# Optimization experiments

Hardware: AMD Instinct MI355X
Metric: run time of the kernel (lower is better)

## Reference

```python
import jax, jax.numpy as jnp
import numpy as np

N_EMBD = 2048
N_HEAD = 16
N_INNER = 8192
EPS = 1e-5


def _wn_weight(v, g):
    # torch weight_norm with dim=1 on weight [out, in]:
    # w[:, j] = g[j] * v[:, j] / ||v[:, j]||_2
    norm = jnp.sqrt(jnp.sum(v * v, axis=0))  # [in]
    return v * (g / norm)[None, :]


def _layer_norm(x, gamma, beta):
    mu = jnp.mean(x, axis=-1, keepdims=True)
    var = jnp.mean(jnp.square(x - mu), axis=-1, keepdims=True)
    return (x - mu) * jax.lax.rsqrt(var + EPS) * gamma + beta


def setup_inputs() -> dict:
    key = jax.random.key(0)
    ks = jax.random.split(key, 12)
    E, I, H = N_EMBD, N_INNER, N_HEAD
    s = lambda n: 1.0 / np.sqrt(n)
    return {
        "hidden_states": jax.random.normal(ks[0], (2, 2048, E), jnp.float32),
        "ln1_g": jnp.ones((E,), jnp.float32),
        "ln1_b": jnp.zeros((E,), jnp.float32),
        "w_qkv": jax.random.normal(ks[1], (3 * E, E), jnp.float32) * s(E),
        "b_qkv": jnp.zeros((3 * E,), jnp.float32),
        "attn_proj_v": jax.random.normal(ks[2], (E, E), jnp.float32) * s(E),
        "attn_proj_g": jnp.abs(jax.random.normal(ks[3], (E,), jnp.float32)) + 0.5,
        "attn_proj_b": jnp.zeros((E,), jnp.float32),
        "emotion_bias": jax.random.normal(ks[4], (H,), jnp.float32) * 0.1,
        "ln2_g": jnp.ones((E,), jnp.float32),
        "ln2_b": jnp.zeros((E,), jnp.float32),
        "w_fc": jax.random.normal(ks[5], (I, E), jnp.float32) * s(E),
        "b_fc": jnp.zeros((I,), jnp.float32),
        "mlp_proj_v": jax.random.normal(ks[6], (E, I), jnp.float32) * s(I),
        "mlp_proj_g": jnp.abs(jax.random.normal(ks[7], (I,), jnp.float32)) + 0.5,
        "mlp_proj_b": jnp.zeros((E,), jnp.float32),
    }


def reference(hidden_states, ln1_g, ln1_b, w_qkv, b_qkv, attn_proj_v, attn_proj_g,
              attn_proj_b, emotion_bias, ln2_g, ln2_b, w_fc, b_fc,
              mlp_proj_v, mlp_proj_g, mlp_proj_b):
    B, S, E = hidden_states.shape
    H = N_HEAD
    D = E // H

    # --- attention sub-block ---
    residual = hidden_states
    x = _layer_norm(hidden_states, ln1_g, ln1_b)
    qkv = x @ w_qkv.T + b_qkv                       # [B,S,3E]
    q, k, v = jnp.split(qkv, 3, axis=-1)
    q = q.reshape(B, S, H, D).transpose(0, 2, 1, 3)  # [B,H,S,D]
    k = k.reshape(B, S, H, D).transpose(0, 2, 1, 3)
    v = v.reshape(B, S, H, D).transpose(0, 2, 1, 3)

    scores = jnp.einsum("bhqd,bhkd->bhqk", q, k) / jnp.sqrt(jnp.float32(D))
    scores = scores + emotion_bias[None, :, None, None]
    probs = jax.nn.softmax(scores, axis=-1)
    attn = jnp.einsum("bhqk,bhkd->bhqd", probs, v)   # [B,H,S,D]
    attn = attn.transpose(0, 2, 1, 3).reshape(B, S, E)
    w_proj = _wn_weight(attn_proj_v, attn_proj_g)
    attn = attn @ w_proj.T + attn_proj_b

    hidden = attn + residual

    # --- MLP sub-block ---
    residual = hidden
    x = _layer_norm(hidden, ln2_g, ln2_b)
    h = jax.nn.gelu(x @ w_fc.T + b_fc, approximate=False)
    w_proj2 = _wn_weight(mlp_proj_v, mlp_proj_g)
    h = h @ w_proj2.T + mlp_proj_b
    return residual + h
```

## Files before the change

kernel.cpp:

```cpp
#include <hip/hip_runtime.h>
#include <hip/hip_bf16.h>

#define DEVI __device__ __forceinline__

typedef __attribute__((ext_vector_type(8))) __bf16 bf16x8;
typedef __attribute__((ext_vector_type(4))) float f32x4;
typedef __attribute__((ext_vector_type(4))) unsigned short u16x4;
typedef __attribute__((ext_vector_type(8))) unsigned short u16x8;

DEVI unsigned short f2bf(float f) {
  unsigned int u = __float_as_uint(f);
  u += 0x7FFFu + ((u >> 16) & 1u);
  return (unsigned short)(u >> 16);
}
DEVI float bf2f(unsigned short u) {
  return __uint_as_float(((unsigned int)u) << 16);
}

#define GLD16(g, l) __builtin_amdgcn_global_load_lds(                      \
    (const __attribute__((address_space(1))) void*)(g),                    \
    (__attribute__((address_space(3))) void*)(l), 16, 0, 0)


__global__ __launch_bounds__(256) void cast_k(const float* __restrict__ in,
                                              unsigned short* __restrict__ out,
                                              int n4) {
  for (int i = blockIdx.x * 256 + threadIdx.x; i < n4; i += gridDim.x * 256) {
    f32x4 v = ((const f32x4*)in)[i];
    u16x4 o;
    o.x = f2bf(v.x); o.y = f2bf(v.y); o.z = f2bf(v.z); o.w = f2bf(v.w);
    ((u16x4*)out)[i] = o;
  }
}

__global__ __launch_bounds__(256) void colnorm1_k(const float* __restrict__ v,
                                                  float* __restrict__ part,
                                                  int cols) {
  const int tid = threadIdx.x;
  const int g = tid & 127;
  const int s = tid >> 7;
  const int c0 = blockIdx.x * 512;
  const int r0 = blockIdx.y * 64 + s * 32;
  const float* base = v + (size_t)r0 * cols + c0 + g * 4;
  f32x4 acc = {};
#pragma unroll 4
  for (int i = 0; i < 32; ++i) {
    f32x4 x = *(const f32x4*)(base + (size_t)i * cols);
    acc.x += x.x * x.x; acc.y += x.y * x.y;
    acc.z += x.z * x.z; acc.w += x.w * x.w;
  }
  __shared__ f32x4 red[256];
  red[tid] = acc;
  __syncthreads();
  if (s == 0) {
    f32x4 a = red[tid], b = red[tid + 128];
    f32x4 o;
    o.x = a.x + b.x; o.y = a.y + b.y; o.z = a.z + b.z; o.w = a.w + b.w;
    *(f32x4*)(part + (size_t)blockIdx.y * cols + c0 + g * 4) = o;
  }
}

__global__ __launch_bounds__(256) void colnorm2_k(const float* __restrict__ part,
                                                  const float* __restrict__ g,
                                                  float* __restrict__ s,
                                                  int cols, int nrc) {
  const int c = blockIdx.x * 256 + threadIdx.x;
  float acc = 0.f;
  for (int i = 0; i < nrc; ++i) acc += part[(size_t)i * cols + c];
  s[c] = g[c] * rsqrtf(acc);
}

__global__ __launch_bounds__(256) void scale_cast_k(const float* __restrict__ in,
                                                    const float* __restrict__ s,
                                                    unsigned short* __restrict__ out,
                                                    int cols, int n4) {
  const int cmask4 = (cols >> 2) - 1;
  for (int i = blockIdx.x * 256 + threadIdx.x; i < n4; i += gridDim.x * 256) {
    f32x4 v = ((const f32x4*)in)[i];
    f32x4 sv = ((const f32x4*)s)[i & cmask4];
    u16x4 o;
    o.x = f2bf(v.x * sv.x); o.y = f2bf(v.y * sv.y);
    o.z = f2bf(v.z * sv.z); o.w = f2bf(v.w * sv.w);
    ((u16x4*)out)[i] = o;
  }
}

__global__ __launch_bounds__(256) void ln_k(const float* __restrict__ x,
                                            const float* __restrict__ g,
                                            const float* __restrict__ b,
                                            unsigned short* __restrict__ out) {
  const int tid = threadIdx.x, lane = tid & 63, wid = tid >> 6;
  const int row = blockIdx.x;
  const float* xr = x + (size_t)row * 2048;
  f32x4 a0 = ((const f32x4*)xr)[tid];
  f32x4 a1 = ((const f32x4*)xr)[tid + 256];
  float s = a0.x + a0.y + a0.z + a0.w + a1.x + a1.y + a1.z + a1.w;
  float ss = a0.x * a0.x + a0.y * a0.y + a0.z * a0.z + a0.w * a0.w +
             a1.x * a1.x + a1.y * a1.y + a1.z * a1.z + a1.w * a1.w;
#pragma unroll
  for (int m = 1; m < 64; m <<= 1) {
    s += __shfl_xor(s, m);
    ss += __shfl_xor(ss, m);
  }
  __shared__ float red[8];
  if (lane == 0) { red[wid] = s; red[4 + wid] = ss; }
  __syncthreads();
  s = red[0] + red[1] + red[2] + red[3];
  ss = red[4] + red[5] + red[6] + red[7];
  const float mu = s * (1.f / 2048.f);
  const float var = ss * (1.f / 2048.f) - mu * mu;
  const float rs = rsqrtf(var + 1e-5f);
  f32x4 g0 = ((const f32x4*)g)[tid], g1 = ((const f32x4*)g)[tid + 256];
  f32x4 b0 = ((const f32x4*)b)[tid], b1 = ((const f32x4*)b)[tid + 256];
  u16x4 o0, o1;
  o0.x = f2bf((a0.x - mu) * rs * g0.x + b0.x);
  o0.y = f2bf((a0.y - mu) * rs * g0.y + b0.y);
  o0.z = f2bf((a0.z - mu) * rs * g0.z + b0.z);
  o0.w = f2bf((a0.w - mu) * rs * g0.w + b0.w);
  o1.x = f2bf((a1.x - mu) * rs * g1.x + b1.x);
  o1.y = f2bf((a1.y - mu) * rs * g1.y + b1.y);
  o1.z = f2bf((a1.z - mu) * rs * g1.z + b1.z);
  o1.w = f2bf((a1.w - mu) * rs * g1.w + b1.w);
  unsigned short* orow = out + (size_t)row * 2048;
  *(u16x4*)(orow + 4 * tid) = o0;
  *(u16x4*)(orow + 1024 + 4 * tid) = o1;
}

__global__ __launch_bounds__(256) void vtrans_k(const unsigned short* __restrict__ qkv,
                                                unsigned short* __restrict__ vt) {
  __shared__ unsigned short t[64][134];
  const int tid = threadIdx.x;
  const int bh = blockIdx.x >> 5, st = blockIdx.x & 31;
  const int b = bh >> 4, h = bh & 15;
  const unsigned short* vb = qkv + (size_t)(b * 2048 + st * 64) * 6144 + 4096 + h * 128;
#pragma unroll
  for (int i = 0; i < 4; ++i) {
    int f = tid + (i << 8);
    int row = f >> 4, c8 = f & 15;
    u16x8 x = *(const u16x8*)(vb + (size_t)row * 6144 + c8 * 8);
#pragma unroll
    for (int j = 0; j < 4; ++j) {
      unsigned int pk = ((unsigned int)x[2 * j + 1] << 16) | x[2 * j];
      *(unsigned int*)&t[row][c8 * 8 + 2 * j] = pk;
    }
  }
  __syncthreads();
  const int lane = tid & 63, wid = tid >> 6;
  unsigned short* ob = vt + ((size_t)bh << 18) + (st << 6);
#pragma unroll
  for (int j = 0; j < 32; ++j) {
    int d = (wid << 5) + j;
    ob[((size_t)d << 11) + lane] = t[lane][d];
  }
}

__global__ __launch_bounds__(256) void g4red_k(const unsigned short* __restrict__ parts,
                                               const float* __restrict__ bias,
                                               const float* __restrict__ res,
                                               float* __restrict__ out, int n4) {
  const size_t PS = (size_t)4096 * 2048;
  for (int i = blockIdx.x * 256 + threadIdx.x; i < n4; i += gridDim.x * 256) {
    u16x4 a = ((const u16x4*)(parts))[i];
    u16x4 b = ((const u16x4*)(parts + PS))[i];
    u16x4 c = ((const u16x4*)(parts + 2 * PS))[i];
    u16x4 d = ((const u16x4*)(parts + 3 * PS))[i];
    f32x4 r = ((const f32x4*)res)[i];
    f32x4 bb = ((const f32x4*)bias)[i & 511];
    f32x4 o;
    o.x = bf2f(a.x) + bf2f(b.x) + bf2f(c.x) + bf2f(d.x) + r.x + bb.x;
    o.y = bf2f(a.y) + bf2f(b.y) + bf2f(c.y) + bf2f(d.y) + r.y + bb.y;
    o.z = bf2f(a.z) + bf2f(b.z) + bf2f(c.z) + bf2f(d.z) + r.z + bb.z;
    o.w = bf2f(a.w) + bf2f(b.w) + bf2f(c.w) + bf2f(d.w) + r.w + bb.w;
    ((f32x4*)out)[i] = o;
  }
}

struct GemmP {
  const unsigned short* A;
  const unsigned short* B;
  const float* bias;
  const float* res;
  float* outF;
  unsigned short* outH;
  int M, N, K;
};

DEVI void gemm128_body(const GemmP& p, int m0, int n0, int k0, int nk) {
  const int tid = threadIdx.x, lane = tid & 63, wid = tid >> 6;
  const int K = p.K;
  const int wr = wid >> 1, wc = wid & 1;

  __shared__ __align__(16) unsigned short sA[2][4096];
  __shared__ __align__(16) unsigned short sB[2][4096];

  const int c0 = tid, c1 = tid + 256;
  const unsigned short* gA0 = p.A + (size_t)(m0 + (c0 >> 2)) * K + k0 + ((c0 & 3) << 3);
  const unsigned short* gA1 = p.A + (size_t)(m0 + (c1 >> 2)) * K + k0 + ((c1 & 3) << 3);
  const unsigned short* gB0 = p.B + (size_t)(n0 + (c0 >> 2)) * K + k0 + ((c0 & 3) << 3);
  const unsigned short* gB1 = p.B + (size_t)(n0 + (c1 >> 2)) * K + k0 + ((c1 & 3) << 3);
  const int l0 = wid << 9, l1 = (wid << 9) + 2048;

  f32x4 acc[4][4] = {};
  const int arow = (wr << 6) + (lane & 15);
  const int brow = (wc << 6) + (lane & 15);
  const int koff = (lane >> 4) << 3;

#define STAGE128(bufi, t) do { int ko = (t) << 5;       \
    GLD16(gA0 + ko, &sA[bufi][l0]);                     \
    GLD16(gA1 + ko, &sA[bufi][l1]);                     \
    GLD16(gB0 + ko, &sB[bufi][l0]);                     \
    GLD16(gB1 + ko, &sB[bufi][l1]); } while (0)

  STAGE128(0, 0);
  __syncthreads();
  int cur = 0;
  for (int t = 0; t < nk; ++t) {
    if (t + 1 < nk) STAGE128(cur ^ 1, t + 1);
    bf16x8 af[4], bfr[4];
#pragma unroll
    for (int i = 0; i < 4; ++i)
      af[i] = *(const bf16x8*)&sA[cur][(arow + (i << 4)) * 32 + koff];
#pragma unroll
    for (int i = 0; i < 4; ++i)
      bfr[i] = *(const bf16x8*)&sB[cur][(brow + (i << 4)) * 32 + koff];
#pragma unroll
    for (int i = 0; i < 4; ++i)
#pragma unroll
      for (int j = 0; j < 4; ++j)
        acc[i][j] = __builtin_amdgcn_mfma_f32_16x16x32_bf16(af[i], bfr[j], acc[i][j], 0, 0, 0);
    __syncthreads();
    cur ^= 1;
  }
#undef STAGE128

  const int rbase = m0 + (wr << 6) + ((lane >> 4) << 2);
  const int cbase = n0 + (wc << 6) + (lane & 15);
#pragma unroll
  for (int mi = 0; mi < 4; ++mi) {
#pragma unroll
    for (int ni = 0; ni < 4; ++ni) {
      const int col = cbase + (ni << 4);
#pragma unroll
      for (int r = 0; r < 4; ++r) {
        const int row = rbase + (mi << 4) + r;
        const size_t o = (size_t)row * p.N + col;
        p.outF[o] = acc[mi][ni][r] + p.bias[col] + p.res[o];
      }
    }
  }
}

__global__ __launch_bounds__(256) void g2_proj128(GemmP p) {
  const int x = blockIdx.x & 7, i = blockIdx.x >> 3;
  const int bm = (x >> 1) * 8 + (i >> 3);
  const int bn = (x & 1) * 8 + (i & 7);
  gemm128_body(p, bm << 7, bn << 7, 0, p.K >> 5);
}

DEVI void setup256(const GemmP& p, int m0, int n0, int k0,
                   const unsigned short*& gsA0, const unsigned short*& gsA1,
                   const unsigned short*& gsB0, const unsigned short*& gsB1) {
  const int tid = threadIdx.x;
  int r_[2], c_[2];
#pragma unroll
  for (int j = 0; j < 2; ++j) {
    int d = tid * 16 + j * 8192;
    int w = (d & 1023) ^ (((d >> 9) & 1) << 5);
    r_[j] = ((d >> 10) << 4) + (w >> 6);
    c_[j] = (w & 63) >> 1;
  }
  gsA0 = p.A + (size_t)(m0 + r_[0]) * p.K + k0 + c_[0];
  gsA1 = p.A + (size_t)(m0 + r_[1]) * p.K + k0 + c_[1];
  gsB0 = p.B + (size_t)(n0 + r_[0]) * p.K + k0 + c_[0];
  gsB1 = p.B + (size_t)(n0 + r_[1]) * p.K + k0 + c_[1];
}

template <int EPI>
DEVI void epi256(const GemmP& p, f32x4 (&acc)[8][4], int m0, int n0,
                 unsigned short* outH) {
  const int lane = threadIdx.x & 63, wid = threadIdx.x >> 6;
  const int wr = wid >> 2, wc = wid & 3;
  const int lr = lane & 15, lk = lane >> 4;
  const int rbase = m0 + wr * 128 + (lk << 2);
  const int cbase = n0 + wc * 64 + lr;
#pragma unroll
  for (int m = 0; m < 8; ++m) {
#pragma unroll
    for (int n = 0; n < 4; ++n) {
      const int col = cbase + (n << 4);
      const float bb = (EPI == 5) ? 0.f : p.bias[col];
#pragma unroll
      for (int r = 0; r < 4; ++r) {
        const int row = rbase + (m << 4) + r;
        float v = acc[m][n][r] + bb;
        if constexpr (EPI == 2) {
          float y = 0.7978845608028654f * (v + 0.044715f * v * v * v);
          float u = __expf(2.f * y);
          v = (y > 40.f) ? v : v * (u / (u + 1.f));
        }
        outH[(size_t)row * p.N + col] = f2bf(v);
      }
    }
  }
}

template <int EPI>
DEVI void gemm2p_body(const GemmP& p, unsigned short* lds_raw, int m0, int n0,
                      int k0, int nk, unsigned short* outH) {
  const int tid = threadIdx.x, lane = tid & 63, wid = tid >> 6;
  const int wr = wid >> 2, wc = wid & 3;
  const int lr = lane & 15, lk = lane >> 4;
  const int fb = (lr * 64 + lk * 16) ^ ((lr & 8) << 2);

  const unsigned short *gsA0, *gsA1, *gsB0, *gsB1;
  setup256(p, m0, n0, k0, gsA0, gsA1, gsB0, gsB1);

#define STG2(b, kt) do { unsigned short* _d = lds_raw + ((b) << 14);     \
    GLD16(gsA0 + ((size_t)(kt) << 5), _d + (tid << 3));                  \
    GLD16(gsA1 + ((size_t)(kt) << 5), _d + 4096 + (tid << 3));           \
    GLD16(gsB0 + ((size_t)(kt) << 5), _d + 8192 + (tid << 3));           \
    GLD16(gsB1 + ((size_t)(kt) << 5), _d + 12288 + (tid << 3)); } while (0)

  f32x4 acc[8][4] = {};
  STG2(0, 0);
  __syncthreads();
  int cur = 0;
  for (int t = 0; t < nk; ++t) {
    if (t + 1 < nk) STG2(cur ^ 1, t + 1);
    const char* tA = (const char*)(lds_raw + (cur << 14));
    const char* tB = tA + 16384;
    bf16x8 a_[8], b_[4];
#pragma unroll
    for (int n = 0; n < 4; ++n)
      b_[n] = *(const bf16x8*)(tB + (((wc << 2) + n) << 10) + fb);
#pragma unroll
    for (int m = 0; m < 8; ++m)
      a_[m] = *(const bf16x8*)(tA + (((wr << 3) + m) << 10) + fb);
#pragma unroll
    for (int m = 0; m < 8; ++m)
#pragma unroll
      for (int n = 0; n < 4; ++n)
        acc[m][n] = __builtin_amdgcn_mfma_f32_16x16x32_bf16(a_[m], b_[n], acc[m][n], 0, 0, 0);
    __syncthreads();
    cur ^= 1;
  }
#undef STG2
  epi256<EPI>(p, acc, m0, n0, outH);
}

template <int EPI>
DEVI void gemmr4_body(const GemmP& p, unsigned short* lds_raw, int m0, int n0,
                      int k0, int nk, unsigned short* outH) {
  const int tid = threadIdx.x, lane = tid & 63, wid = tid >> 6;
  const int wr = wid >> 2, wc = wid & 3;
  const int lr = lane & 15, lk = lane >> 4;
  const int fb = (lr * 64 + lk * 16) ^ ((lr & 8) << 2);

  const unsigned short *gsA0, *gsA1, *gsB0, *gsB1;
  setup256(p, m0, n0, k0, gsA0, gsA1, gsB0, gsB1);

#define STGR(bufi, kt) do { unsigned short* _d = lds_raw + ((bufi) << 14); \
    GLD16(gsA0 + ((size_t)(kt) << 5), _d + (tid << 3));                    \
    GLD16(gsA1 + ((size_t)(kt) << 5), _d + 4096 + (tid << 3));             \
    GLD16(gsB0 + ((size_t)(kt) << 5), _d + 8192 + (tid << 3));             \
    GLD16(gsB1 + ((size_t)(kt) << 5), _d + 12288 + (tid << 3)); } while (0)

  f32x4 acc[8][4] = {};
  STGR(0, 0);
  STGR(1, 1);
  STGR(2, 2);
  asm volatile("s_waitcnt vmcnt(8)" ::: "memory");
  __builtin_amdgcn_s_barrier();
  asm volatile("" ::: "memory");

  for (int t = 0; t < nk; ++t) {
    const char* tA = (const char*)(lds_raw + ((t & 3) << 14));
    const char* tB = tA + 16384;
    bf16x8 a_[8], b_[4];
#pragma unroll
    for (int n = 0; n < 4; ++n)
      b_[n] = *(const bf16x8*)(tB + (((wc << 2) + n) << 10) + fb);
#pragma unroll
    for (int m = 0; m < 8; ++m)
      a_[m] = *(const bf16x8*)(tA + (((wr << 3) + m) << 10) + fb);
    if (t + 3 < nk) STGR((t + 3) & 3, t + 3);
    __builtin_amdgcn_s_setprio(1);
#pragma unroll
    for (int m = 0; m < 8; ++m)
#pragma unroll
      for (int n = 0; n < 4; ++n)
        acc[m][n] = __builtin_amdgcn_mfma_f32_16x16x32_bf16(a_[m], b_[n], acc[m][n], 0, 0, 0);
    __builtin_amdgcn_s_setprio(0);
    if (t + 3 < nk)      asm volatile("s_waitcnt vmcnt(8)" ::: "memory");
    else if (t + 2 < nk) asm volatile("s_waitcnt vmcnt(4)" ::: "memory");
    else if (t + 1 < nk) asm volatile("s_waitcnt vmcnt(0)" ::: "memory");
    __builtin_amdgcn_s_barrier();
    asm volatile("" ::: "memory");
  }
#undef STGR
  epi256<EPI>(p, acc, m0, n0, outH);
}

__global__ __launch_bounds__(512, 2) void g1_qkv256(GemmP p) {
  extern __shared__ unsigned short lds_raw[];
  const int x = blockIdx.x & 7, i = blockIdx.x >> 3;
  const int bm = (x & 1) * 8 + (i & 7);
  const int bn = (x >> 1) * 6 + (i >> 3);
  gemm2p_body<0>(p, lds_raw, bm << 8, bn << 8, 0, p.K >> 5, p.outH);
}
__global__ __launch_bounds__(512, 1) void g3_fc256r4(GemmP p) {
  extern __shared__ unsigned short lds_raw[];
  const int x = blockIdx.x & 7, i = blockIdx.x >> 3;
  const int bm = (x & 1) * 8 + (i & 7);
  const int bn = (x >> 1) * 8 + (i >> 3);
  gemmr4_body<2>(p, lds_raw, bm << 8, bn << 8, 0, p.K >> 5, p.outH);
}
__global__ __launch_bounds__(512, 1) void g4_splitk256r4(GemmP p) {
  extern __shared__ unsigned short lds_raw[];
  const int x = blockIdx.x & 7, i = blockIdx.x >> 3;
  const int ks = x & 3;
  const int bm = (x >> 2) * 8 + (i >> 3);
  const int bn = i & 7;
  unsigned short* outH = p.outH + (size_t)ks * 4096 * 2048;
  gemmr4_body<5>(p, lds_raw, bm << 8, bn << 8, ks << 11, 64, outH);
}

__global__ __launch_bounds__(512) void attn_k(const unsigned short* __restrict__ qkv,
                                              const unsigned short* __restrict__ Vt,
                                              unsigned short* __restrict__ O) {
  const int tid = threadIdx.x, lane = tid & 63, wid = tid >> 6;
  const int bid = blockIdx.x;
  const int pos = bid >> 3;
  const int bh = (bid & 7) * 4 + (pos >> 4);
  const int qt = pos & 15;
  const int q0 = qt * 128 + wid * 16;
  const int b = bh >> 4, h = bh & 15;

  __shared__ __align__(16) unsigned short sK[64 * 128];
  __shared__ __align__(16) unsigned short sV[128 * 64];
  __shared__ __align__(16) unsigned short sP[8][16 * 72];

  const unsigned short* Qb = qkv + (size_t)(b * 2048) * 6144 + h * 128;
  const unsigned short* Kb = qkv + (size_t)(b * 2048) * 6144 + 2048 + h * 128;
  const unsigned short* Vb = Vt + ((size_t)bh << 18);

  bf16x8 qf[4];
  {
    const unsigned short* qp = Qb + (size_t)(q0 + (lane & 15)) * 6144 + ((lane >> 4) << 3);
#pragma unroll
    for (int kk = 0; kk < 4; ++kk) qf[kk] = *(const bf16x8*)(qp + kk * 32);
  }

  int koffs[2], voffs[2];
#pragma unroll
  for (int i = 0; i < 2; ++i) {
    const int c = tid + (i << 9);
    const int kv = c >> 4, jj = c & 15;
    const int js = (jj & 8) | ((jj ^ kv) & 7);
    koffs[i] = kv * 6144 + (js << 3);
    const int d = c >> 3, j2 = c & 7;
    const int js2 = j2 ^ (d & 7);
    voffs[i] = d * 2048 + (js2 << 3);
  }
  u16x8 kreg[2], vreg[2];
  auto PREF = [&](int kt) {
    const int kv0 = kt << 6;
    const unsigned short* kb = Kb + (size_t)kv0 * 6144;
#pragma unroll
    for (int i = 0; i < 2; ++i) {
      kreg[i] = *(const u16x8*)(kb + koffs[i]);
      vreg[i] = *(const u16x8*)(Vb + kv0 + voffs[i]);
    }
  };

  f32x4 oacc[8] = {};
  float mrun = -3e38f, lrun = 0.f;
  PREF(0);

  for (int kt = 0; kt < 32; ++kt) {
#pragma unroll
    for (int i = 0; i < 2; ++i) {
      const int c8 = (tid + (i << 9)) << 3;
      *(u16x8*)&sK[c8] = kreg[i];
      *(u16x8*)&sV[c8] = vreg[i];
    }
    __syncthreads();
    if (kt + 1 < 32) PREF(kt + 1);

    f32x4 sc[4] = {};
    __builtin_amdgcn_s_setprio(1);
#pragma unroll
    for (int ti = 0; ti < 4; ++ti) {
#pragma unroll
      for (int kk = 0; kk < 4; ++kk) {
        const int row = (ti << 4) + (lane & 15);
        int bo = (row << 8) + (kk << 6) + ((lane >> 4) << 4);
        bo ^= (row & 7) << 4;
        bf16x8 kf = *(const bf16x8*)((const char*)sK + bo);
        sc[ti] = __builtin_amdgcn_mfma_f32_16x16x32_bf16(kf, qf[kk], sc[ti], 0, 0, 0);
      }
    }
    __builtin_amdgcn_s_setprio(0);

    float pv[16];
    float mx = -3e38f;
#pragma unroll
    for (int ti = 0; ti < 4; ++ti)
#pragma unroll
      for (int r = 0; r < 4; ++r) {
        float x = sc[ti][r] * 0.08838834764831845f;
        pv[(ti << 2) + r] = x;
        mx = fmaxf(mx, x);
      }
    mx = fmaxf(mx, __shfl_xor(mx, 16));
    mx = fmaxf(mx, __shfl_xor(mx, 32));

    float corr = 1.f;
    if (!__all(mx - mrun <= 8.f)) {
      const float mnew = fmaxf(mrun, mx);
      corr = __expf(mrun - mnew);
      mrun = mnew;
      float fr[4];
#pragma unroll
      for (int r = 0; r < 4; ++r) fr[r] = __shfl(corr, ((lane >> 4) << 2) + r);
#pragma unroll
      for (int di = 0; di < 8; ++di)
#pragma unroll
        for (int r = 0; r < 4; ++r) oacc[di][r] *= fr[r];
    }
    float psum = 0.f;
#pragma unroll
    for (int i2 = 0; i2 < 16; ++i2) {
      float e = __expf(pv[i2] - mrun);
      pv[i2] = e;
      psum += e;
    }
    psum += __shfl_xor(psum, 16);
    psum += __shfl_xor(psum, 32);
    lrun = lrun * corr + psum;

    unsigned short* prow = &sP[wid][(lane & 15) * 72];
#pragma unroll
    for (int ti = 0; ti < 4; ++ti) {
      u16x4 w4;
      w4.x = f2bf(pv[(ti << 2) + 0]);
      w4.y = f2bf(pv[(ti << 2) + 1]);
      w4.z = f2bf(pv[(ti << 2) + 2]);
      w4.w = f2bf(pv[(ti << 2) + 3]);
      *(u16x4*)&prow[(ti << 4) + ((lane >> 4) << 2)] = w4;
    }

    __builtin_amdgcn_s_setprio(1);
#pragma unroll
    for (int di = 0; di < 8; ++di) {
#pragma unroll
      for (int ks = 0; ks < 2; ++ks) {
        bf16x8 pf = *(const bf16x8*)((const char*)&sP[wid][0] +
                                     (lane & 15) * 144 + (ks << 6) + ((lane >> 4) << 4));
        const int dr = (di << 4) + (lane & 15);
        int bo = (dr << 7) + (ks << 6) + ((lane >> 4) << 4);
        bo ^= (dr & 7) << 4;
        bf16x8 vf = *(const bf16x8*)((const char*)sV + bo);
        oacc[di] = __builtin_amdgcn_mfma_f32_16x16x32_bf16(pf, vf, oacc[di], 0, 0, 0);
      }
    }
    __builtin_amdgcn_s_setprio(0);
    __syncthreads();
  }

  float il[4];
#pragma unroll
  for (int r = 0; r < 4; ++r) il[r] = 1.f / __shfl(lrun, ((lane >> 4) << 2) + r);
  const size_t obase = ((size_t)(b * 2048 + q0)) * 2048 + h * 128;
#pragma unroll
  for (int di = 0; di < 8; ++di)
#pragma unroll
    for (int r = 0; r < 4; ++r) {
      const size_t o = obase + (size_t)(((lane >> 4) << 2) + r) * 2048 + (di << 4) + (lane & 15);
      O[o] = f2bf(oacc[di][r] * il[r]);
    }
}


extern "C" void kernel_launch(void* const* d_in, const int* in_sizes, int n_in,
                              void* d_out, int out_size, void* d_ws, size_t ws_size,
                              hipStream_t stream) {
  (void)in_sizes; (void)n_in; (void)out_size; (void)ws_size;
  const float* hidden = (const float*)d_in[0];
  const float* ln1_g = (const float*)d_in[1];
  const float* ln1_b = (const float*)d_in[2];
  const float* w_qkv = (const float*)d_in[3];
  const float* b_qkv = (const float*)d_in[4];
  const float* apv = (const float*)d_in[5];
  const float* apg = (const float*)d_in[6];
  const float* apb = (const float*)d_in[7];
  const float* ln2_g = (const float*)d_in[9];
  const float* ln2_b = (const float*)d_in[10];
  const float* w_fc = (const float*)d_in[11];
  const float* b_fc = (const float*)d_in[12];
  const float* mpv = (const float*)d_in[13];
  const float* mpg = (const float*)d_in[14];
  const float* mpb = (const float*)d_in[15];

  char* w = (char*)d_ws;
  const size_t MBs = 1ull << 20;
  unsigned short* xln = (unsigned short*)(w + 0);
  float* hidden2 = (float*)(w + 0);
  unsigned short* vtbuf = (unsigned short*)(w + 32 * MBs);
  unsigned short* hbuf = (unsigned short*)(w + 32 * MBs);
  unsigned short* qkv = (unsigned short*)(w + 96 * MBs);
  unsigned short* wfc_bf = (unsigned short*)(w + 96 * MBs);
  unsigned short* partH = (unsigned short*)(w + 96 * MBs);
  unsigned short* xln2 = (unsigned short*)(w + 128 * MBs);
  unsigned short* attn_out = (unsigned short*)(w + 144 * MBs);
  unsigned short* wqkv_bf = (unsigned short*)(w + 160 * MBs);
  unsigned short* w2_bf = (unsigned short*)(w + 160 * MBs);
  unsigned short* wproj_bf = (unsigned short*)(w + 192 * MBs);
  float* s_attn = (float*)(w + 200 * MBs);
  float* s_mlp = (float*)(w + 200 * MBs + 32768);
  float* part_attn = (float*)(w + 201 * MBs);
  float* part_mlp = (float*)(w + 202 * MBs);

  hipFuncSetAttribute((const void*)g1_qkv256, hipFuncAttributeMaxDynamicSharedMemorySize, 65536);
  hipFuncSetAttribute((const void*)g3_fc256r4, hipFuncAttributeMaxDynamicSharedMemorySize, 131072);
  hipFuncSetAttribute((const void*)g4_splitk256r4, hipFuncAttributeMaxDynamicSharedMemorySize, 131072);

  cast_k<<<2048, 256, 0, stream>>>(w_qkv, wqkv_bf, (6144 * 2048) / 4);
  colnorm1_k<<<dim3(4, 32), 256, 0, stream>>>(apv, part_attn, 2048);
  colnorm2_k<<<8, 256, 0, stream>>>(part_attn, apg, s_attn, 2048, 32);
  scale_cast_k<<<2048, 256, 0, stream>>>(apv, s_attn, wproj_bf, 2048, (2048 * 2048) / 4);
  colnorm1_k<<<dim3(16, 32), 256, 0, stream>>>(mpv, part_mlp, 8192);
  colnorm2_k<<<32, 256, 0, stream>>>(part_mlp, mpg, s_mlp, 8192, 32);

  ln_k<<<4096, 256, 0, stream>>>(hidden, ln1_g, ln1_b, xln);

  GemmP p1 = {xln, wqkv_bf, b_qkv, nullptr, nullptr, qkv, 4096, 6144, 2048};
  g1_qkv256<<<384, 512, 65536, stream>>>(p1);

  vtrans_k<<<1024, 256, 0, stream>>>(qkv, vtbuf);

  attn_k<<<512, 512, 0, stream>>>(qkv, vtbuf, attn_out);

  cast_k<<<2048, 256, 0, stream>>>(w_fc, wfc_bf, (8192 * 2048) / 4);
  scale_cast_k<<<4096, 256, 0, stream>>>(mpv, s_mlp, w2_bf, 8192, (2048 * 8192) / 4);

  GemmP p2 = {attn_out, wproj_bf, apb, hidden, hidden2, nullptr, 4096, 2048, 2048};
  g2_proj128<<<512, 256, 0, stream>>>(p2);

  ln_k<<<4096, 256, 0, stream>>>(hidden2, ln2_g, ln2_b, xln2);

  GemmP p3 = {xln2, wfc_bf, b_fc, nullptr, nullptr, hbuf, 4096, 8192, 2048};
  g3_fc256r4<<<512, 512, 131072, stream>>>(p3);

  GemmP p4 = {hbuf, w2_bf, mpb, nullptr, nullptr, partH, 4096, 2048, 8192};
  g4_splitk256r4<<<512, 512, 131072, stream>>>(p4);
  g4red_k<<<2048, 256, 0, stream>>>(partH, mpb, hidden2, (float*)d_out,
                                    (4096 * 2048) / 4);
}
```

Before: 750.5 us.

## Use K=64 double-buffered GEMM stages and exp2-based softmax in attention

New measurement: 735.8 us. About the same (-2.0%).

```diff
diff --git a/kernel.cpp b/kernel.cpp
--- a/kernel.cpp
+++ b/kernel.cpp
@@ -349,8 +349,8 @@
 }
 
 template <int EPI>
-DEVI void gemmr4_body(const GemmP& p, unsigned short* lds_raw, int m0, int n0,
-                      int k0, int nk, unsigned short* outH) {
+DEVI void gemmr2k64_body(const GemmP& p, unsigned short* lds_raw, int m0, int n0,
+                         int k0, int nk64, unsigned short* outH) {
   const int tid = threadIdx.x, lane = tid & 63, wid = tid >> 6;
   const int wr = wid >> 2, wc = wid & 3;
   const int lr = lane & 15, lk = lane >> 4;
@@ -359,45 +359,50 @@
   const unsigned short *gsA0, *gsA1, *gsB0, *gsB1;
   setup256(p, m0, n0, k0, gsA0, gsA1, gsB0, gsB1);
 
-#define STGR(bufi, kt) do { unsigned short* _d = lds_raw + ((bufi) << 14); \
-    GLD16(gsA0 + ((size_t)(kt) << 5), _d + (tid << 3));                    \
-    GLD16(gsA1 + ((size_t)(kt) << 5), _d + 4096 + (tid << 3));             \
-    GLD16(gsB0 + ((size_t)(kt) << 5), _d + 8192 + (tid << 3));             \
-    GLD16(gsB1 + ((size_t)(kt) << 5), _d + 12288 + (tid << 3)); } while (0)
+#define STG64(bufi, kt) do { unsigned short* _d = lds_raw + ((bufi) << 15);  \
+    int _ko = (kt) << 6;                                                     \
+    GLD16(gsA0 + _ko,      _d + (tid << 3));                                 \
+    GLD16(gsA1 + _ko,      _d + 4096 + (tid << 3));                          \
+    GLD16(gsA0 + _ko + 32, _d + 8192 + (tid << 3));                          \
+    GLD16(gsA1 + _ko + 32, _d + 12288 + (tid << 3));                         \
+    GLD16(gsB0 + _ko,      _d + 16384 + (tid << 3));                         \
+    GLD16(gsB1 + _ko,      _d + 20480 + (tid << 3));                         \
+    GLD16(gsB0 + _ko + 32, _d + 24576 + (tid << 3));                         \
+    GLD16(gsB1 + _ko + 32, _d + 28672 + (tid << 3)); } while (0)
 
   f32x4 acc[8][4] = {};
-  STGR(0, 0);
-  STGR(1, 1);
-  STGR(2, 2);
-  asm volatile("s_waitcnt vmcnt(8)" ::: "memory");
+  STG64(0, 0);
+  asm volatile("s_waitcnt vmcnt(0)" ::: "memory");
   __builtin_amdgcn_s_barrier();
   asm volatile("" ::: "memory");
 
-  for (int t = 0; t < nk; ++t) {
-    const char* tA = (const char*)(lds_raw + ((t & 3) << 14));
-    const char* tB = tA + 16384;
-    bf16x8 a_[8], b_[4];
-#pragma unroll
-    for (int n = 0; n < 4; ++n)
-      b_[n] = *(const bf16x8*)(tB + (((wc << 2) + n) << 10) + fb);
-#pragma unroll
-    for (int m = 0; m < 8; ++m)
-      a_[m] = *(const bf16x8*)(tA + (((wr << 3) + m) << 10) + fb);
-    if (t + 3 < nk) STGR((t + 3) & 3, t + 3);
-    __builtin_amdgcn_s_setprio(1);
-#pragma unroll
-    for (int m = 0; m < 8; ++m)
+  for (int t = 0; t < nk64; ++t) {
+    if (t + 1 < nk64) STG64((t + 1) & 1, t + 1);
+    const char* base = (const char*)(lds_raw + ((t & 1) << 15));
+#pragma unroll
+    for (int s = 0; s < 2; ++s) {
+      const char* tA = base + s * 16384;
+      const char* tB = base + 32768 + s * 16384;
+      bf16x8 a_[8], b_[4];
 #pragma unroll
       for (int n = 0; n < 4; ++n)
-        acc[m][n] = __builtin_amdgcn_mfma_f32_16x16x32_bf16(a_[m], b_[n], acc[m][n], 0, 0, 0);
-    __builtin_amdgcn_s_setprio(0);
-    if (t + 3 < nk)      asm volatile("s_waitcnt vmcnt(8)" ::: "memory");
-    else if (t + 2 < nk) asm volatile("s_waitcnt vmcnt(4)" ::: "memory");
-    else if (t + 1 < nk) asm volatile("s_waitcnt vmcnt(0)" ::: "memory");
+        b_[n] = *(const bf16x8*)(tB + (((wc << 2) + n) << 10) + fb);
+#pragma unroll
+      for (int m = 0; m < 8; ++m)
+        a_[m] = *(const bf16x8*)(tA + (((wr << 3) + m) << 10) + fb);
+      __builtin_amdgcn_s_setprio(1);
+#pragma unroll
+      for (int m = 0; m < 8; ++m)
+#pragma unroll
+        for (int n = 0; n < 4; ++n)
+          acc[m][n] = __builtin_amdgcn_mfma_f32_16x16x32_bf16(a_[m], b_[n], acc[m][n], 0, 0, 0);
+      __builtin_amdgcn_s_setprio(0);
+    }
+    if (t + 1 < nk64) asm volatile("s_waitcnt vmcnt(0)" ::: "memory");
     __builtin_amdgcn_s_barrier();
     asm volatile("" ::: "memory");
   }
-#undef STGR
+#undef STG64
   epi256<EPI>(p, acc, m0, n0, outH);
 }
 
@@ -408,21 +413,21 @@
   const int bn = (x >> 1) * 6 + (i >> 3);
   gemm2p_body<0>(p, lds_raw, bm << 8, bn << 8, 0, p.K >> 5, p.outH);
 }
-__global__ __launch_bounds__(512, 1) void g3_fc256r4(GemmP p) {
+__global__ __launch_bounds__(512, 1) void g3_fc64(GemmP p) {
   extern __shared__ unsigned short lds_raw[];
   const int x = blockIdx.x & 7, i = blockIdx.x >> 3;
   const int bm = (x & 1) * 8 + (i & 7);
   const int bn = (x >> 1) * 8 + (i >> 3);
-  gemmr4_body<2>(p, lds_raw, bm << 8, bn << 8, 0, p.K >> 5, p.outH);
-}
-__global__ __launch_bounds__(512, 1) void g4_splitk256r4(GemmP p) {
+  gemmr2k64_body<2>(p, lds_raw, bm << 8, bn << 8, 0, 32, p.outH);
+}
+__global__ __launch_bounds__(512, 1) void g4_sk64(GemmP p) {
   extern __shared__ unsigned short lds_raw[];
   const int x = blockIdx.x & 7, i = blockIdx.x >> 3;
   const int ks = x & 3;
   const int bm = (x >> 2) * 8 + (i >> 3);
   const int bn = i & 7;
   unsigned short* outH = p.outH + (size_t)ks * 4096 * 2048;
-  gemmr4_body<5>(p, lds_raw, bm << 8, bn << 8, ks << 11, 64, outH);
+  gemmr2k64_body<5>(p, lds_raw, bm << 8, bn << 8, ks << 11, 32, outH);
 }
 
 __global__ __launch_bounds__(512) void attn_k(const unsigned short* __restrict__ qkv,
@@ -435,6 +440,7 @@
   const int qt = pos & 15;
   const int q0 = qt * 128 + wid * 16;
   const int b = bh >> 4, h = bh & 15;
+  const float C = 0.08838834764831845f * 1.4426950408889634f;
 
   __shared__ __align__(16) unsigned short sK[64 * 128];
   __shared__ __align__(16) unsigned short sV[128 * 64];
@@ -508,7 +514,7 @@
     for (int ti = 0; ti < 4; ++ti)
 #pragma unroll
       for (int r = 0; r < 4; ++r) {
-        float x = sc[ti][r] * 0.08838834764831845f;
+        float x = sc[ti][r];
         pv[(ti << 2) + r] = x;
         mx = fmaxf(mx, x);
       }
@@ -516,9 +522,9 @@
     mx = fmaxf(mx, __shfl_xor(mx, 32));
 
     float corr = 1.f;
-    if (!__all(mx - mrun <= 8.f)) {
+    if (!__all(mx - mrun <= 90.50966799f)) {
       const float mnew = fmaxf(mrun, mx);
-      corr = __expf(mrun - mnew);
+      corr = exp2f((mrun - mnew) * C);
       mrun = mnew;
       float fr[4];
 #pragma unroll
@@ -531,7 +537,7 @@
     float psum = 0.f;
 #pragma unroll
     for (int i2 = 0; i2 < 16; ++i2) {
-      float e = __expf(pv[i2] - mrun);
+      float e = exp2f((pv[i2] - mrun) * C);
       pv[i2] = e;
       psum += e;
     }
@@ -550,18 +556,22 @@
       *(u16x4*)&prow[(ti << 4) + ((lane >> 4) << 2)] = w4;
     }
 
+    bf16x8 pfA, pfB;
+    {
+      const char* pb = (const char*)&sP[wid][0] + (lane & 15) * 144 + ((lane >> 4) << 4);
+      pfA = *(const bf16x8*)(pb);
+      pfB = *(const bf16x8*)(pb + 64);
+    }
     __builtin_amdgcn_s_setprio(1);
 #pragma unroll
     for (int di = 0; di < 8; ++di) {
 #pragma unroll
       for (int ks = 0; ks < 2; ++ks) {
-        bf16x8 pf = *(const bf16x8*)((const char*)&sP[wid][0] +
-                                     (lane & 15) * 144 + (ks << 6) + ((lane >> 4) << 4));
         const int dr = (di << 4) + (lane & 15);
         int bo = (dr << 7) + (ks << 6) + ((lane >> 4) << 4);
         bo ^= (dr & 7) << 4;
         bf16x8 vf = *(const bf16x8*)((const char*)sV + bo);
-        oacc[di] = __builtin_amdgcn_mfma_f32_16x16x32_bf16(pf, vf, oacc[di], 0, 0, 0);
+        oacc[di] = __builtin_amdgcn_mfma_f32_16x16x32_bf16(ks ? pfB : pfA, vf, oacc[di], 0, 0, 0);
       }
     }
     __builtin_amdgcn_s_setprio(0);
@@ -622,8 +632,8 @@
   float* part_mlp = (float*)(w + 202 * MBs);
 
   hipFuncSetAttribute((const void*)g1_qkv256, hipFuncAttributeMaxDynamicSharedMemorySize, 65536);
-  hipFuncSetAttribute((const void*)g3_fc256r4, hipFuncAttributeMaxDynamicSharedMemorySize, 131072);
-  hipFuncSetAttribute((const void*)g4_splitk256r4, hipFuncAttributeMaxDynamicSharedMemorySize, 131072);
+  hipFuncSetAttribute((const void*)g3_fc64, hipFuncAttributeMaxDynamicSharedMemorySize, 131072);
+  hipFuncSetAttribute((const void*)g4_sk64, hipFuncAttributeMaxDynamicSharedMemorySize, 131072);
 
   cast_k<<<2048, 256, 0, stream>>>(w_qkv, wqkv_bf, (6144 * 2048) / 4);
   colnorm1_k<<<dim3(4, 32), 256, 0, stream>>>(apv, part_attn, 2048);
@@ -650,10 +660,10 @@
   ln_k<<<4096, 256, 0, stream>>>(hidden2, ln2_g, ln2_b, xln2);
 
   GemmP p3 = {xln2, wfc_bf, b_fc, nullptr, nullptr, hbuf, 4096, 8192, 2048};
-  g3_fc256r4<<<512, 512, 131072, stream>>>(p3);
+  g3_fc64<<<512, 512, 131072, stream>>>(p3);
 
   GemmP p4 = {hbuf, w2_bf, mpb, nullptr, nullptr, partH, 4096, 2048, 8192};
-  g4_splitk256r4<<<512, 512, 131072, stream>>>(p4);
+  g4_sk64<<<512, 512, 131072, stream>>>(p4);
   g4red_k<<<2048, 256, 0, stream>>>(partH, mpb, hidden2, (float*)d_out,
                                     (4096 * 2048) / 4);
 }
```
